# Kernel tuning notes

Measured on AMD Instinct MI355X. Metric: run time of the kernel, lower is better.

The kernel has to match this reference:

```python
import jax, jax.numpy as jnp
import numpy as np

N = 50000      # nodes
E = 800000     # edges (pos and neg each)
IN = 128       # in_channels
HID = 64       # hidden_dim
H = 4          # heads
OUT = 64       # out_channels


def setup_inputs() -> dict:
    key = jax.random.key(0)
    ks = jax.random.split(key, 11)
    s = 0.05
    return {
        "x": jax.random.normal(ks[0], (N, IN), dtype=jnp.float32),
        "pos_edge_index": jax.random.randint(ks[1], (2, E), 0, N, dtype=jnp.int32),
        "neg_edge_index": jax.random.randint(ks[2], (2, E), 0, N, dtype=jnp.int32),
        # conv1 params: Linear [IN, H*HID], attention vectors [H, HID], bias [H*HID]
        "W1": jax.random.normal(ks[3], (IN, H * HID), dtype=jnp.float32) * s,
        "att_src1": jax.random.normal(ks[4], (H, HID), dtype=jnp.float32) * s,
        "att_dst1": jax.random.normal(ks[5], (H, HID), dtype=jnp.float32) * s,
        "b1": jax.random.normal(ks[6], (H * HID,), dtype=jnp.float32) * s,
        # conv2 params: heads=1
        "W2": jax.random.normal(ks[7], (H * HID, OUT), dtype=jnp.float32) * s,
        "att_src2": jax.random.normal(ks[8], (1, OUT), dtype=jnp.float32) * s,
        "att_dst2": jax.random.normal(ks[9], (1, OUT), dtype=jnp.float32) * s,
        "b2": jax.random.normal(ks[10], (OUT,), dtype=jnp.float32) * s,
    }


def gat_conv(x, edge_index, W, att_src, att_dst, bias, heads, ch):
    """PyG GATConv: add self-loops, per-head linear, leaky-relu edge score,
    scatter-softmax over target neighborhoods, scatter-add aggregation."""
    n = x.shape[0]
    loop = jnp.arange(n, dtype=edge_index.dtype)
    src = jnp.concatenate([edge_index[0], loop])  # message source j
    dst = jnp.concatenate([edge_index[1], loop])  # aggregation target i

    h = (x @ W).reshape(n, heads, ch)                      # [N, H, C]
    a_s = jnp.einsum("nhc,hc->nh", h, att_src)             # alpha from source
    a_d = jnp.einsum("nhc,hc->nh", h, att_dst)             # alpha from target

    alpha = jax.nn.leaky_relu(a_s[src] + a_d[dst], 0.2)    # [Etot, H]
    m = jax.ops.segment_max(alpha, dst, num_segments=n)    # per-target max
    e = jnp.exp(alpha - m[dst])
    denom = jax.ops.segment_sum(e, dst, num_segments=n)
    w = e / (denom[dst] + 1e-16)                           # softmax weights

    out = jax.ops.segment_sum(w[:, :, None] * h[src], dst, num_segments=n)
    return out.reshape(n, heads * ch) + bias


def reference(x, pos_edge_index, neg_edge_index,
              W1, att_src1, att_dst1, b1,
              W2, att_src2, att_dst2, b2):
    # encode
    z = jax.nn.relu(gat_conv(x, pos_edge_index, W1, att_src1, att_dst1, b1, H, HID))
    z = gat_conv(z, pos_edge_index, W2, att_src2, att_dst2, b2, 1, OUT)
    # decode: edge dot-product logits over pos + neg edges
    ei = jnp.concatenate([pos_edge_index, neg_edge_index], axis=-1)  # [2, 2E]
    logits = (z[ei[0]] * z[ei[1]]).sum(axis=-1)                      # [2E]
    return logits
```

## Files before the change

### kernel.cpp

```cpp
#include <hip/hip_runtime.h>
#include <hip/hip_bf16.h>
#include <math.h>

#define IN_CH 128
#define HID 64
#define HEADS 4
#define C1 (HEADS*HID)
#define OUT_CH 64
#define NSL 64
#define MAXNH 25024

typedef __attribute__((ext_vector_type(8))) short short8v;
typedef __attribute__((ext_vector_type(4))) float f32x4;

__device__ __forceinline__ float lrelu(float x){ return x > 0.f ? x : 0.2f*x; }

__device__ __forceinline__ ushort f2b(float f){
  unsigned u = __builtin_bit_cast(unsigned, f);
  unsigned r = (u + 0x7FFF + ((u>>16)&1)) >> 16;
  return (ushort)r;
}
__device__ __forceinline__ float b2f(ushort b){
  unsigned u = ((unsigned)b) << 16;
  return __builtin_bit_cast(float, u);
}

__device__ __forceinline__ float wsum64(float v){
  #pragma unroll
  for (int m = 32; m >= 1; m >>= 1) v += __shfl_xor(v, m, 64);
  return v;
}

__device__ __forceinline__ float dot2(unsigned ua, unsigned ub){
  float la = __builtin_bit_cast(float, ua << 16);
  float ha = __builtin_bit_cast(float, ua & 0xFFFF0000u);
  float lb = __builtin_bit_cast(float, ub << 16);
  float hb = __builtin_bit_cast(float, ub & 0xFFFF0000u);
  return la*lb + ha*hb;
}

__device__ __forceinline__ void unpack8(uint4 u, float* v){
  v[0]=__builtin_bit_cast(float,u.x<<16); v[1]=__builtin_bit_cast(float,u.x&0xFFFF0000u);
  v[2]=__builtin_bit_cast(float,u.y<<16); v[3]=__builtin_bit_cast(float,u.y&0xFFFF0000u);
  v[4]=__builtin_bit_cast(float,u.z<<16); v[5]=__builtin_bit_cast(float,u.z&0xFFFF0000u);
  v[6]=__builtin_bit_cast(float,u.w<<16); v[7]=__builtin_bit_cast(float,u.w&0xFFFF0000u);
}


__global__ __launch_bounds__(1024) void k_hist2(
    const int* __restrict__ dst, unsigned* __restrict__ part, int e, int nh, int n){
  __shared__ unsigned hist[MAXNH];
  int b = blockIdx.x;
  int half = b >> 6, slice = b & (NSL-1);
  int base = half*nh;
  int cnt = half ? (n - nh) : nh;
  int tid = threadIdx.x;
  for (int i = tid; i < cnt; i += 1024) hist[i] = 0u;
  __syncthreads();
  int ES = (e + NSL - 1) / NSL;
  int es = slice*ES, ee = min(e, es + ES);
  for (int t = es + tid; t < ee; t += 1024){
    int d = dst[t];
    if (d >= base && d < base + cnt) atomicAdd(&hist[d - base], 1u);
  }
  __syncthreads();
  unsigned* pb = part + (size_t)b*nh;
  for (int i = tid; i < cnt; i += 1024) pb[i] = hist[i];
}

__global__ void k_degred(unsigned* __restrict__ part, int* __restrict__ deg,
                         int* __restrict__ bsum, int n, int nh){
  __shared__ int buf[256];
  int b = blockIdx.x, tid = threadIdx.x;
  int g = b*256 + tid;
  int dv = 0;
  if (g < n){
    int half = (g >= nh) ? 1 : 0;
    int i = g - half*nh;
    size_t base = (size_t)(half*NSL)*nh + i;
    unsigned run = 0;
    #pragma unroll 8
    for (int s = 0; s < NSL; ++s){
      unsigned v = part[base + (size_t)s*nh];
      part[base + (size_t)s*nh] = run;
      run += v;
    }
    dv = (int)run + 1;
    deg[g] = dv;
  }
  buf[tid] = dv;
  __syncthreads();
  for (int off = 128; off > 0; off >>= 1){
    if (tid < off) buf[tid] += buf[tid + off];
    __syncthreads();
  }
  if (tid == 0) bsum[b] = buf[0];
}

__global__ void k_scanb(int* bsum, int nb){
  __shared__ int buf[256];
  int tid = threadIdx.x;
  int v = (tid < nb) ? bsum[tid] : 0;
  buf[tid] = v;
  __syncthreads();
  for (int off = 1; off < 256; off <<= 1){
    int t = (tid >= off) ? buf[tid - off] : 0;
    __syncthreads();
    buf[tid] += t;
    __syncthreads();
  }
  if (tid < nb) bsum[tid] = buf[tid] - v;
}

__global__ void k_scanfinal(const int* __restrict__ deg, const int* __restrict__ bsum,
                            int* rowptr, ushort* csrc, int n){
  __shared__ int buf[256];
  int b = blockIdx.x, tid = threadIdx.x;
  int i = b*256 + tid;
  int v = (i < n) ? deg[i] : 0;
  buf[tid] = v;
  __syncthreads();
  for (int off = 1; off < 256; off <<= 1){
    int t = (tid >= off) ? buf[tid - off] : 0;
    __syncthreads();
    buf[tid] += t;
    __syncthreads();
  }
  if (i < n){
    int r = bsum[b] + buf[tid];
    rowptr[i + 1] = r;
    csrc[r - 1] = (ushort)i;
  }
  if (b == 0 && tid == 0) rowptr[0] = 0;
}

__global__ __launch_bounds__(1024) void k_scatter2(
    const int* __restrict__ src, const int* __restrict__ dst,
    const int* __restrict__ rowptr, const unsigned* __restrict__ part,
    ushort* __restrict__ csrc, int e, int nh, int n){
  __shared__ unsigned cur[MAXNH];
  int b = blockIdx.x;
  int half = b >> 6, slice = b & (NSL-1);
  int base = half*nh;
  int cnt = half ? (n - nh) : nh;
  int tid = threadIdx.x;
  const unsigned* pb = part + (size_t)b*nh;
  for (int i = tid; i < cnt; i += 1024)
    cur[i] = (unsigned)rowptr[base + i] + pb[i];
  __syncthreads();
  int ES = (e + NSL - 1) / NSL;
  int es = slice*ES, ee = min(e, es + ES);
  for (int t = es + tid; t < ee; t += 1024){
    int d = dst[t];
    if (d >= base && d < base + cnt){
      unsigned slot = atomicAdd(&cur[d - base], 1u);
      __builtin_nontemporal_store((ushort)src[t], csrc + slot);
    }
  }
}

__global__ void k_setup(const float* __restrict__ W1, ushort* __restrict__ W1t,
                        const float* __restrict__ W2, ushort* __restrict__ W2t,
                        const float* __restrict__ as1v, const float* __restrict__ ad1v,
                        const float* __restrict__ as2v, const float* __restrict__ ad2v,
                        float* was4, float* wad4, float* w2s, float* w2d){
  int b = blockIdx.x, tid = threadIdx.x;
  if (b < 128){
    int i = b*256 + tid;
    int k = i >> 8, c = i & 255;
    W1t[(size_t)c*IN_CH + k] = f2b(W1[i]);
  } else if (b < 192){
    int i = (b - 128)*256 + tid;
    int k = i >> 6, c = i & 63;
    W2t[(size_t)c*C1 + k] = f2b(W2[i]);
  } else if (b == 192){
    #pragma unroll
    for (int r = 0; r < 2; ++r){
      int t = tid + r*256;
      int c = t >> 2, h = t & 3;
      float s = 0.f, d = 0.f;
      for (int j = 0; j < HID; ++j){
        float w = W1[c*C1 + h*HID + j];
        s += w * as1v[h*HID + j];
        d += w * ad1v[h*HID + j];
      }
      was4[t] = s; wad4[t] = d;
    }
  } else {
    float s = 0.f, d = 0.f;
    for (int o = 0; o < OUT_CH; ++o){
      float w = W2[tid*OUT_CH + o];
      s += w * as2v[o];
      d += w * ad2v[o];
    }
    w2s[tid] = s; w2d[tid] = d;
  }
}

__global__ __launch_bounds__(256) void k_fattc(const float* __restrict__ x,
    const float* __restrict__ was4, const float* __restrict__ wad4,
    ushort* __restrict__ xb, float* __restrict__ as1, float* __restrict__ ad1, int n){
  int i = blockIdx.x*4 + (threadIdx.x >> 6);
  int l = threadIdx.x & 63;
  if (i >= n) return;
  float2 u = *(const float2*)(x + (size_t)i*IN_CH + 2*l);
  ushort2 o; o.x = f2b(u.x); o.y = f2b(u.y);
  *(ushort2*)(xb + (size_t)i*IN_CH + 2*l) = o;
  float v0 = u.x, v1 = u.y;
  f32x4 s0 = *(const f32x4*)(was4 + 8*l);
  f32x4 s1 = *(const f32x4*)(was4 + 8*l + 4);
  f32x4 d0 = *(const f32x4*)(wad4 + 8*l);
  f32x4 d1 = *(const f32x4*)(wad4 + 8*l + 4);
  f32x4 ps, pd;
  #pragma unroll
  for (int h = 0; h < 4; ++h){
    ps[h] = wsum64(v0*s0[h] + v1*s1[h]);
    pd[h] = wsum64(v0*d0[h] + v1*d1[h]);
  }
  if (l == 0){
    *(f32x4*)(as1 + 4*i) = ps;
    *(f32x4*)(ad1 + 4*i) = pd;
  }
}

__global__ __launch_bounds__(256) void k_fatt2(const ushort* __restrict__ z1b,
    const float* __restrict__ w2s, const float* __restrict__ w2d,
    float* __restrict__ as2, float* __restrict__ ad2, int n){
  int i = blockIdx.x*4 + (threadIdx.x >> 6);
  int l = threadIdx.x & 63;
  if (i >= n) return;
  ushort4 u = *(const ushort4*)(z1b + (size_t)i*C1 + 4*l);
  float v0 = b2f(u.x), v1 = b2f(u.y), v2 = b2f(u.z), v3 = b2f(u.w);
  f32x4 s = *(const f32x4*)(w2s + 4*l);
  f32x4 d = *(const f32x4*)(w2d + 4*l);
  float ps = wsum64(v0*s[0] + v1*s[1] + v2*s[2] + v3*s[3]);
  float pd = wsum64(v0*d[0] + v1*d[1] + v2*d[2] + v3*d[3]);
  if (l == 0){ as2[i] = ps; ad2[i] = pd; }
}

__global__ __launch_bounds__(64) void k_fagg1(
    const ushort* __restrict__ xb, const float* __restrict__ as1,
    const float* __restrict__ ad1, const int* __restrict__ rowptr,
    const ushort* __restrict__ csrc, ushort* __restrict__ xagg, int n)
{
  __shared__ float  s_w[4][4][17];
  __shared__ ushort s_src[4][16];
  int tid = threadIdx.x;
  int grp = tid >> 4, ln = tid & 15;
  int i = blockIdx.x*4 + grp;
  if (i >= n) return;
  int beg = rowptr[i], end = rowptr[i+1];
  f32x4 ad4 = *(const f32x4*)(ad1 + 4*i);

  f32x4 S = (f32x4)(0.f);
  f32x4 ev0 = (f32x4)(0.f), ev1 = (f32x4)(0.f);
  int sj0 = 0, sj1 = 0, it = 0;
  for (int sl = beg + ln; sl < end; sl += 16, ++it){
    int sj = csrc[sl];
    f32x4 a4 = *(const f32x4*)(as1 + 4*sj);
    f32x4 ev;
    #pragma unroll
    for (int h = 0; h < 4; ++h)
      ev[h] = __expf(fminf(lrelu(a4[h] + ad4[h]), 60.f));
    if (it == 0){ ev0 = ev; sj0 = sj; }
    else if (it == 1){ ev1 = ev; sj1 = sj; }
    #pragma unroll
    for (int h = 0; h < 4; ++h) S[h] += ev[h];
  }
  f32x4 rd;
  #pragma unroll
  for (int h = 0; h < 4; ++h){
    float sh = S[h];
    #pragma unroll
    for (int k = 8; k >= 1; k >>= 1) sh += __shfl_xor(sh, k, 16);
    rd[h] = 1.f/(sh + 1e-16f);
  }

  float acc[4][8] = {};
  int nch = (end - beg + 15) >> 4;
  for (int c = 0; c < nch; ++c){
    int cs = beg + c*16;
    int cn = min(16, end - cs);
    if (ln < cn){
      int sj; f32x4 ev;
      if (c == 0){ sj = sj0; ev = ev0; }
      else if (c == 1){ sj = sj1; ev = ev1; }
      else {
        sj = csrc[cs + ln];
        f32x4 a4 = *(const f32x4*)(as1 + 4*sj);
        #pragma unroll
        for (int h = 0; h < 4; ++h)
          ev[h] = __expf(fminf(lrelu(a4[h] + ad4[h]), 60.f));
      }
      s_src[grp][ln] = (ushort)sj;
      #pragma unroll
      for (int h = 0; h < 4; ++h)
        s_w[grp][h][ln] = ev[h] * rd[h];
    }
    int e = 0;
    if (cn >= 4){
      uint4 u0 = *(const uint4*)(xb + (size_t)s_src[grp][0]*IN_CH + ln*8);
      uint4 u1 = *(const uint4*)(xb + (size_t)s_src[grp][1]*IN_CH + ln*8);
      uint4 u2 = *(const uint4*)(xb + (size_t)s_src[grp][2]*IN_CH + ln*8);
      uint4 u3 = *(const uint4*)(xb + (size_t)s_src[grp][3]*IN_CH + ln*8);
      for (; e + 7 < cn; e += 4){
        uint4 n0 = *(const uint4*)(xb + (size_t)s_src[grp][e+4]*IN_CH + ln*8);
        uint4 n1 = *(const uint4*)(xb + (size_t)s_src[grp][e+5]*IN_CH + ln*8);
        uint4 n2 = *(const uint4*)(xb + (size_t)s_src[grp][e+6]*IN_CH + ln*8);
        uint4 n3 = *(const uint4*)(xb + (size_t)s_src[grp][e+7]*IN_CH + ln*8);
        float v0[8], v1[8], v2[8], v3[8];
        unpack8(u0, v0); unpack8(u1, v1); unpack8(u2, v2); unpack8(u3, v3);
        #pragma unroll
        for (int h = 0; h < 4; ++h){
          float w0 = s_w[grp][h][e],   w1 = s_w[grp][h][e+1];
          float w2 = s_w[grp][h][e+2], w3 = s_w[grp][h][e+3];
          #pragma unroll
          for (int cc = 0; cc < 8; ++cc)
            acc[h][cc] += w0*v0[cc] + w1*v1[cc] + w2*v2[cc] + w3*v3[cc];
        }
        u0 = n0; u1 = n1; u2 = n2; u3 = n3;
      }
      {
        float v0[8], v1[8], v2[8], v3[8];
        unpack8(u0, v0); unpack8(u1, v1); unpack8(u2, v2); unpack8(u3, v3);
        #pragma unroll
        for (int h = 0; h < 4; ++h){
          float w0 = s_w[grp][h][e],   w1 = s_w[grp][h][e+1];
          float w2 = s_w[grp][h][e+2], w3 = s_w[grp][h][e+3];
          #pragma unroll
          for (int cc = 0; cc < 8; ++cc)
            acc[h][cc] += w0*v0[cc] + w1*v1[cc] + w2*v2[cc] + w3*v3[cc];
        }
        e += 4;
      }
    }
    for (; e < cn; ++e){
      uint4 u = *(const uint4*)(xb + (size_t)s_src[grp][e]*IN_CH + ln*8);
      float v[8];
      unpack8(u, v);
      #pragma unroll
      for (int h = 0; h < 4; ++h){
        float w = s_w[grp][h][e];
        #pragma unroll
        for (int cc = 0; cc < 8; ++cc) acc[h][cc] += w*v[cc];
      }
    }
  }
  #pragma unroll
  for (int h = 0; h < 4; ++h){
    uint4 o;
    o.x = (unsigned)f2b(acc[h][0]) | ((unsigned)f2b(acc[h][1])<<16);
    o.y = (unsigned)f2b(acc[h][2]) | ((unsigned)f2b(acc[h][3])<<16);
    o.z = (unsigned)f2b(acc[h][4]) | ((unsigned)f2b(acc[h][5])<<16);
    o.w = (unsigned)f2b(acc[h][6]) | ((unsigned)f2b(acc[h][7])<<16);
    *(uint4*)(xagg + (size_t)i*512 + h*128 + ln*8) = o;
  }
}

__global__ __launch_bounds__(64) void k_fagg2(
    const ushort* __restrict__ h2b, const float* __restrict__ as2,
    const float* __restrict__ ad2, const int* __restrict__ rowptr,
    const ushort* __restrict__ csrc, const float* __restrict__ bias,
    ushort* __restrict__ z2b, int n)
{
  __shared__ float  s_w[4][17];
  __shared__ ushort s_src[4][16];
  int tid = threadIdx.x;
  int grp = tid >> 4, ln = tid & 15;
  int i = blockIdx.x*4 + grp;
  if (i >= n) return;
  int beg = rowptr[i], end = rowptr[i+1];
  float adv = ad2[i];

  float S = 0.f;
  float ev0 = 0.f, ev1 = 0.f;
  int sj0 = 0, sj1 = 0, it = 0;
  for (int sl = beg + ln; sl < end; sl += 16, ++it){
    int sj = csrc[sl];
    float ev = __expf(fminf(lrelu(as2[sj] + adv), 60.f));
    if (it == 0){ ev0 = ev; sj0 = sj; }
    else if (it == 1){ ev1 = ev; sj1 = sj; }
    S += ev;
  }
  #pragma unroll
  for (int k = 8; k >= 1; k >>= 1) S += __shfl_xor(S, k, 16);
  float rd = 1.f/(S + 1e-16f);

  float acc[4] = {};
  int nch = (end - beg + 15) >> 4;
  for (int c = 0; c < nch; ++c){
    int cs = beg + c*16;
    int cn = min(16, end - cs);
    if (ln < cn){
      int sj; float ev;
      if (c == 0){ sj = sj0; ev = ev0; }
      else if (c == 1){ sj = sj1; ev = ev1; }
      else { sj = csrc[cs + ln]; ev = __expf(fminf(lrelu(as2[sj] + adv), 60.f)); }
      s_src[grp][ln] = (ushort)sj;
      s_w[grp][ln] = ev * rd;
    }
    int e = 0;
    for (; e + 1 < cn; e += 2){
      int sjA = s_src[grp][e], sjB = s_src[grp][e+1];
      float wA = s_w[grp][e], wB = s_w[grp][e+1];
      ushort4 uA = *(const ushort4*)(h2b + (size_t)sjA*OUT_CH + ln*4);
      ushort4 uB = *(const ushort4*)(h2b + (size_t)sjB*OUT_CH + ln*4);
      acc[0] += wA*b2f(uA.x) + wB*b2f(uB.x);
      acc[1] += wA*b2f(uA.y) + wB*b2f(uB.y);
      acc[2] += wA*b2f(uA.z) + wB*b2f(uB.z);
      acc[3] += wA*b2f(uA.w) + wB*b2f(uB.w);
    }
    if (e < cn){
      int sj = s_src[grp][e];
      float w = s_w[grp][e];
      ushort4 u = *(const ushort4*)(h2b + (size_t)sj*OUT_CH + ln*4);
      acc[0] += w*b2f(u.x); acc[1] += w*b2f(u.y);
      acc[2] += w*b2f(u.z); acc[3] += w*b2f(u.w);
    }
  }
  ushort4 o;
  o.x = f2b(acc[0] + bias[ln*4]);
  o.y = f2b(acc[1] + bias[ln*4+1]);
  o.z = f2b(acc[2] + bias[ln*4+2]);
  o.w = f2b(acc[3] + bias[ln*4+3]);
  *(ushort4*)(z2b + (size_t)i*OUT_CH + ln*4) = o;
}

template<bool RELU_BIAS>
__global__ __launch_bounds__(256) void k_gemm2(
    const ushort* __restrict__ A, const ushort* __restrict__ Bt,
    ushort* __restrict__ Cb, const float* __restrict__ bias,
    int M, int K, int lda, int ldc, int aZ, int bZ, int cZ)
{
  constexpr int BM = 128, BN = 64, NF = 2;
  __shared__ uint4 As[BM*8];
  __shared__ uint4 Bs[BN*8];
  int tid = threadIdx.x;
  int wave = tid >> 6, lane = tid & 63;
  int wr = wave >> 1, wc = wave & 1;
  int bm = blockIdx.y * BM;
  int z = blockIdx.z;
  const ushort* Az = A + (size_t)z*aZ;
  const ushort* Bz = Bt + (size_t)z*bZ;
  int g = lane >> 4, lr = lane & 15;

  f32x4 acc[4][NF];
  #pragma unroll
  for (int m = 0; m < 4; ++m)
    #pragma unroll
    for (int n = 0; n < NF; ++n) acc[m][n] = (f32x4)(0.f);

  for (int k0 = 0; k0 < K; k0 += 64){
    for (int idx = tid; idx < BM*8; idx += 256){
      int r = idx >> 3, c = idx & 7;
      int gr = bm + r;
      uint4 v = make_uint4(0u,0u,0u,0u);
      if (gr < M) v = *(const uint4*)(Az + (size_t)gr*lda + k0 + c*8);
      As[r*8 + (c ^ (r & 7))] = v;
    }
    for (int idx = tid; idx < BN*8; idx += 256){
      int r = idx >> 3, c = idx & 7;
      uint4 v = *(const uint4*)(Bz + (size_t)r*K + k0 + c*8);
      Bs[r*8 + (c ^ (r & 7))] = v;
    }
    __syncthreads();
    #pragma unroll
    for (int kk = 0; kk < 2; ++kk){
      short8v af[4], bf[NF];
      #pragma unroll
      for (int m = 0; m < 4; ++m){
        int r = wr*64 + m*16 + lr;
        int c = kk*4 + g;
        af[m] = *(const short8v*)&As[r*8 + (c ^ (r & 7))];
      }
      #pragma unroll
      for (int n = 0; n < NF; ++n){
        int r = wc*32 + n*16 + lr;
        int c = kk*4 + g;
        bf[n] = *(const short8v*)&Bs[r*8 + (c ^ (r & 7))];
      }
      #pragma unroll
      for (int m = 0; m < 4; ++m)
        #pragma unroll
        for (int n = 0; n < NF; ++n)
          acc[m][n] = __builtin_amdgcn_mfma_f32_16x16x32_bf16(af[m], bf[n], acc[m][n], 0, 0, 0);
    }
    __syncthreads();
  }
  #pragma unroll
  for (int m = 0; m < 4; ++m){
    #pragma unroll
    for (int q = 0; q < 4; ++q){
      int row = bm + wr*64 + m*16 + g*4 + q;
      if (row < M){
        #pragma unroll
        for (int n = 0; n < NF; ++n){
          int col = wc*32 + n*16 + lr;
          float v = acc[m][n][q];
          if (RELU_BIAS) v = fmaxf(v + bias[cZ*z + col], 0.f);
          Cb[(size_t)row*ldc + cZ*z + col] = f2b(v);
        }
      }
    }
  }
}

__global__ void k_decode(const ushort* __restrict__ z2b, const int* __restrict__ pos,
                         const int* __restrict__ neg, float* __restrict__ out, int e){
  int g = blockIdx.x*256 + threadIdx.x;
  int hf = e >> 1;
  int k = g >> 3;
  int sub = g & 7;
  if (k >= hf) return;
  int a0 = __builtin_nontemporal_load(pos + k);
  int b0 = __builtin_nontemporal_load(pos + e + k);
  int a1 = __builtin_nontemporal_load(pos + k + hf);
  int b1 = __builtin_nontemporal_load(pos + e + k + hf);
  int a2 = __builtin_nontemporal_load(neg + k);
  int b2 = __builtin_nontemporal_load(neg + e + k);
  int a3 = __builtin_nontemporal_load(neg + k + hf);
  int b3 = __builtin_nontemporal_load(neg + e + k + hf);
  uint4 ua0 = *(const uint4*)(z2b + (size_t)a0*OUT_CH + sub*8);
  uint4 ub0 = *(const uint4*)(z2b + (size_t)b0*OUT_CH + sub*8);
  uint4 ua1 = *(const uint4*)(z2b + (size_t)a1*OUT_CH + sub*8);
  uint4 ub1 = *(const uint4*)(z2b + (size_t)b1*OUT_CH + sub*8);
  uint4 ua2 = *(const uint4*)(z2b + (size_t)a2*OUT_CH + sub*8);
  uint4 ub2 = *(const uint4*)(z2b + (size_t)b2*OUT_CH + sub*8);
  uint4 ua3 = *(const uint4*)(z2b + (size_t)a3*OUT_CH + sub*8);
  uint4 ub3 = *(const uint4*)(z2b + (size_t)b3*OUT_CH + sub*8);
  float p0 = dot2(ua0.x, ub0.x) + dot2(ua0.y, ub0.y) + dot2(ua0.z, ub0.z) + dot2(ua0.w, ub0.w);
  float p1 = dot2(ua1.x, ub1.x) + dot2(ua1.y, ub1.y) + dot2(ua1.z, ub1.z) + dot2(ua1.w, ub1.w);
  float p2 = dot2(ua2.x, ub2.x) + dot2(ua2.y, ub2.y) + dot2(ua2.z, ub2.z) + dot2(ua2.w, ub2.w);
  float p3 = dot2(ua3.x, ub3.x) + dot2(ua3.y, ub3.y) + dot2(ua3.z, ub3.z) + dot2(ua3.w, ub3.w);
  #pragma unroll
  for (int mm = 4; mm >= 1; mm >>= 1){
    p0 += __shfl_xor(p0, mm, 64);
    p1 += __shfl_xor(p1, mm, 64);
    p2 += __shfl_xor(p2, mm, 64);
    p3 += __shfl_xor(p3, mm, 64);
  }
  if (sub == 0){
    __builtin_nontemporal_store(p0, out + k);
    __builtin_nontemporal_store(p1, out + k + hf);
    __builtin_nontemporal_store(p2, out + e + k);
    __builtin_nontemporal_store(p3, out + e + k + hf);
  }
}

extern "C" void kernel_launch(void* const* d_in, const int* in_sizes, int n_in,
                              void* d_out, int out_size, void* d_ws, size_t ws_size,
                              hipStream_t stream) {
  const float* x        = (const float*)d_in[0];
  const int*   pos      = (const int*)d_in[1];
  const int*   neg      = (const int*)d_in[2];
  const float* W1       = (const float*)d_in[3];
  const float* att_src1 = (const float*)d_in[4];
  const float* att_dst1 = (const float*)d_in[5];
  const float* b1       = (const float*)d_in[6];
  const float* W2       = (const float*)d_in[7];
  const float* att_src2 = (const float*)d_in[8];
  const float* att_dst2 = (const float*)d_in[9];
  const float* b2       = (const float*)d_in[10];
  float* out = (float*)d_out;

  const int N = in_sizes[0] / IN_CH;
  const int E = in_sizes[1] / 2;
  const int NNZ = E + N;
  const int NH = (N + 1) / 2;

  char* w = (char*)d_ws;
  ushort* xb   = (ushort*)w;  w += (size_t)N*IN_CH*2;
  ushort* xagg = (ushort*)w;  w += (size_t)N*512*2;
  ushort* z1b  = (ushort*)w;  w += (size_t)N*C1*2;
  float* as1   = (float*)w;   w += (size_t)N*4*4;
  float* ad1   = (float*)w;   w += (size_t)N*4*4;
  float* as2   = (float*)w;   w += (size_t)N*4;
  float* ad2   = (float*)w;   w += (size_t)N*4;
  ushort* W1t  = (ushort*)w;  w += (size_t)C1*IN_CH*2;
  ushort* W2t  = (ushort*)w;  w += (size_t)OUT_CH*C1*2;
  float* was4  = (float*)w;   w += 512*4;
  float* wad4  = (float*)w;   w += 512*4;
  float* w2s   = (float*)w;   w += 256*4;
  float* w2d   = (float*)w;   w += 256*4;
  int* deg     = (int*)w;     w += (size_t)N*4;
  int* rowptr  = (int*)w;     w += (size_t)(N+1)*4;
  int* bsum    = (int*)w;     w += (size_t)256*4;
  unsigned* part = (unsigned*)w; w += (size_t)2*NSL*NH*4;
  ushort* csrc = (ushort*)w;  w += (size_t)NNZ*2;

  ushort* h2b = xagg;
  ushort* z2b = xagg + (size_t)N*OUT_CH;

  int nb = (N + 255)/256;
  const int* pdst = pos + E;

  k_setup<<<194, 256, 0, stream>>>(W1, W1t, W2, W2t,
      att_src1, att_dst1, att_src2, att_dst2, was4, wad4, w2s, w2d);
  k_hist2<<<2*NSL, 1024, 0, stream>>>(pdst, part, E, NH, N);
  k_degred<<<nb, 256, 0, stream>>>(part, deg, bsum, N, NH);
  k_fattc<<<(N + 3)/4, 256, 0, stream>>>(x, was4, wad4, xb, as1, ad1, N);
  k_scanb<<<1, 256, 0, stream>>>(bsum, nb);
  k_scanfinal<<<nb, 256, 0, stream>>>(deg, bsum, rowptr, csrc, N);
  k_scatter2<<<2*NSL, 1024, 0, stream>>>(pos, pdst, rowptr, part, csrc, E, NH, N);

  k_fagg1<<<(N + 3)/4, 64, 0, stream>>>(xb, as1, ad1, rowptr, csrc, xagg, N);

  {
    dim3 g(1, (N + 127)/128, 4);
    k_gemm2<true><<<g, 256, 0, stream>>>(xagg, W1t, z1b, b1,
        N, IN_CH, 512, C1, IN_CH, OUT_CH*IN_CH, OUT_CH);
  }
  k_fatt2<<<(N + 3)/4, 256, 0, stream>>>(z1b, w2s, w2d, as2, ad2, N);

  {
    dim3 g(1, (N + 127)/128, 1);
    k_gemm2<false><<<g, 256, 0, stream>>>(z1b, W2t, h2b, nullptr,
        N, C1, C1, OUT_CH, 0, 0, 0);
  }
  k_fagg2<<<(N + 3)/4, 64, 0, stream>>>(h2b, as2, ad2, rowptr, csrc, b2, z2b, N);

  int db = (int)(((size_t)(E/2)*8 + 255)/256);
  k_decode<<<db, 256, 0, stream>>>(z2b, pos, neg, out, E);
}
```

Before: 243.6 us.

## Split CSR build into quarter-node partitions, fold block scan, prefetch agg loads

The histogram and scatter kernels now split the node range into four quarters instead of two. This shrinks each block's shared-memory table, which should allow more resident blocks, and doubles the block count. The separate single-block scan of block sums is removed: each scanfinal block now sums the preceding block totals itself, which saves a kernel launch at the cost of redundant reads. The second-layer aggregation loop software-pipelines its gathered feature loads one pair ahead to hide memory latency. A side effect is that every edge is now read by four blocks instead of two.

Result: no change. 240.0 us (-1.5%).

```diff
diff --git a/kernel.cpp b/kernel.cpp
--- a/kernel.cpp
+++ b/kernel.cpp
@@ -8,7 +8,8 @@
 #define C1 (HEADS*HID)
 #define OUT_CH 64
 #define NSL 64
-#define MAXNH 25024
+#define NQ 4
+#define MAXNQ 12512
 
 typedef __attribute__((ext_vector_type(8))) short short8v;
 typedef __attribute__((ext_vector_type(4))) float f32x4;
@@ -48,12 +49,12 @@
 
 
 __global__ __launch_bounds__(1024) void k_hist2(
-    const int* __restrict__ dst, unsigned* __restrict__ part, int e, int nh, int n){
-  __shared__ unsigned hist[MAXNH];
+    const int* __restrict__ dst, unsigned* __restrict__ part, int e, int nq, int n){
+  __shared__ unsigned hist[MAXNQ];
   int b = blockIdx.x;
-  int half = b >> 6, slice = b & (NSL-1);
-  int base = half*nh;
-  int cnt = half ? (n - nh) : nh;
+  int q = b >> 6, slice = b & (NSL-1);
+  int base = q*nq;
+  int cnt = min(nq, n - base);
   int tid = threadIdx.x;
   for (int i = tid; i < cnt; i += 1024) hist[i] = 0u;
   __syncthreads();
@@ -64,25 +65,25 @@
     if (d >= base && d < base + cnt) atomicAdd(&hist[d - base], 1u);
   }
   __syncthreads();
-  unsigned* pb = part + (size_t)b*nh;
+  unsigned* pb = part + (size_t)b*nq;
   for (int i = tid; i < cnt; i += 1024) pb[i] = hist[i];
 }
 
 __global__ void k_degred(unsigned* __restrict__ part, int* __restrict__ deg,
-                         int* __restrict__ bsum, int n, int nh){
+                         int* __restrict__ bsum, int n, int nq){
   __shared__ int buf[256];
   int b = blockIdx.x, tid = threadIdx.x;
   int g = b*256 + tid;
   int dv = 0;
   if (g < n){
-    int half = (g >= nh) ? 1 : 0;
-    int i = g - half*nh;
-    size_t base = (size_t)(half*NSL)*nh + i;
+    int q = g / nq;
+    int i = g - q*nq;
+    size_t base = (size_t)(q*NSL)*nq + i;
     unsigned run = 0;
     #pragma unroll 8
     for (int s = 0; s < NSL; ++s){
-      unsigned v = part[base + (size_t)s*nh];
-      part[base + (size_t)s*nh] = run;
+      unsigned v = part[base + (size_t)s*nq];
+      part[base + (size_t)s*nq] = run;
       run += v;
     }
     dv = (int)run + 1;
@@ -97,25 +98,23 @@
   if (tid == 0) bsum[b] = buf[0];
 }
 
-__global__ void k_scanb(int* bsum, int nb){
-  __shared__ int buf[256];
-  int tid = threadIdx.x;
-  int v = (tid < nb) ? bsum[tid] : 0;
-  buf[tid] = v;
-  __syncthreads();
-  for (int off = 1; off < 256; off <<= 1){
-    int t = (tid >= off) ? buf[tid - off] : 0;
-    __syncthreads();
-    buf[tid] += t;
-    __syncthreads();
-  }
-  if (tid < nb) bsum[tid] = buf[tid] - v;
-}
-
 __global__ void k_scanfinal(const int* __restrict__ deg, const int* __restrict__ bsum,
                             int* rowptr, ushort* csrc, int n){
   __shared__ int buf[256];
+  __shared__ int s_base;
   int b = blockIdx.x, tid = threadIdx.x;
+  int part = 0;
+  for (int s = tid; s < b; s += 256) part += bsum[s];
+  buf[tid] = part;
+  __syncthreads();
+  for (int off = 128; off > 0; off >>= 1){
+    if (tid < off) buf[tid] += buf[tid + off];
+    __syncthreads();
+  }
+  if (tid == 0) s_base = buf[0];
+  __syncthreads();
+  int base = s_base;
+
   int i = b*256 + tid;
   int v = (i < n) ? deg[i] : 0;
   buf[tid] = v;
@@ -127,7 +126,7 @@
     __syncthreads();
   }
   if (i < n){
-    int r = bsum[b] + buf[tid];
+    int r = base + buf[tid];
     rowptr[i + 1] = r;
     csrc[r - 1] = (ushort)i;
   }
@@ -137,14 +136,14 @@
 __global__ __launch_bounds__(1024) void k_scatter2(
     const int* __restrict__ src, const int* __restrict__ dst,
     const int* __restrict__ rowptr, const unsigned* __restrict__ part,
-    ushort* __restrict__ csrc, int e, int nh, int n){
-  __shared__ unsigned cur[MAXNH];
+    ushort* __restrict__ csrc, int e, int nq, int n){
+  __shared__ unsigned cur[MAXNQ];
   int b = blockIdx.x;
-  int half = b >> 6, slice = b & (NSL-1);
-  int base = half*nh;
-  int cnt = half ? (n - nh) : nh;
+  int q = b >> 6, slice = b & (NSL-1);
+  int base = q*nq;
+  int cnt = min(nq, n - base);
   int tid = threadIdx.x;
-  const unsigned* pb = part + (size_t)b*nh;
+  const unsigned* pb = part + (size_t)b*nq;
   for (int i = tid; i < cnt; i += 1024)
     cur[i] = (unsigned)rowptr[base + i] + pb[i];
   __syncthreads();
@@ -400,15 +399,27 @@
       s_w[grp][ln] = ev * rd;
     }
     int e = 0;
-    for (; e + 1 < cn; e += 2){
-      int sjA = s_src[grp][e], sjB = s_src[grp][e+1];
-      float wA = s_w[grp][e], wB = s_w[grp][e+1];
-      ushort4 uA = *(const ushort4*)(h2b + (size_t)sjA*OUT_CH + ln*4);
-      ushort4 uB = *(const ushort4*)(h2b + (size_t)sjB*OUT_CH + ln*4);
-      acc[0] += wA*b2f(uA.x) + wB*b2f(uB.x);
-      acc[1] += wA*b2f(uA.y) + wB*b2f(uB.y);
-      acc[2] += wA*b2f(uA.z) + wB*b2f(uB.z);
-      acc[3] += wA*b2f(uA.w) + wB*b2f(uB.w);
+    if (cn >= 2){
+      ushort4 uA = *(const ushort4*)(h2b + (size_t)s_src[grp][0]*OUT_CH + ln*4);
+      ushort4 uB = *(const ushort4*)(h2b + (size_t)s_src[grp][1]*OUT_CH + ln*4);
+      for (; e + 3 < cn; e += 2){
+        ushort4 uC = *(const ushort4*)(h2b + (size_t)s_src[grp][e+2]*OUT_CH + ln*4);
+        ushort4 uD = *(const ushort4*)(h2b + (size_t)s_src[grp][e+3]*OUT_CH + ln*4);
+        float wA = s_w[grp][e], wB = s_w[grp][e+1];
+        acc[0] += wA*b2f(uA.x) + wB*b2f(uB.x);
+        acc[1] += wA*b2f(uA.y) + wB*b2f(uB.y);
+        acc[2] += wA*b2f(uA.z) + wB*b2f(uB.z);
+        acc[3] += wA*b2f(uA.w) + wB*b2f(uB.w);
+        uA = uC; uB = uD;
+      }
+      {
+        float wA = s_w[grp][e], wB = s_w[grp][e+1];
+        acc[0] += wA*b2f(uA.x) + wB*b2f(uB.x);
+        acc[1] += wA*b2f(uA.y) + wB*b2f(uB.y);
+        acc[2] += wA*b2f(uA.z) + wB*b2f(uB.z);
+        acc[3] += wA*b2f(uA.w) + wB*b2f(uB.w);
+        e += 2;
+      }
     }
     if (e < cn){
       int sj = s_src[grp][e];
@@ -566,7 +577,7 @@
   const int N = in_sizes[0] / IN_CH;
   const int E = in_sizes[1] / 2;
   const int NNZ = E + N;
-  const int NH = (N + 1) / 2;
+  const int NQ4 = (N + NQ - 1) / NQ;
 
   char* w = (char*)d_ws;
   ushort* xb   = (ushort*)w;  w += (size_t)N*IN_CH*2;
@@ -585,7 +596,7 @@
   int* deg     = (int*)w;     w += (size_t)N*4;
   int* rowptr  = (int*)w;     w += (size_t)(N+1)*4;
   int* bsum    = (int*)w;     w += (size_t)256*4;
-  unsigned* part = (unsigned*)w; w += (size_t)2*NSL*NH*4;
+  unsigned* part = (unsigned*)w; w += (size_t)NQ*NSL*NQ4*4;
   ushort* csrc = (ushort*)w;  w += (size_t)NNZ*2;
 
   ushort* h2b = xagg;
@@ -596,12 +607,11 @@
 
   k_setup<<<194, 256, 0, stream>>>(W1, W1t, W2, W2t,
       att_src1, att_dst1, att_src2, att_dst2, was4, wad4, w2s, w2d);
-  k_hist2<<<2*NSL, 1024, 0, stream>>>(pdst, part, E, NH, N);
-  k_degred<<<nb, 256, 0, stream>>>(part, deg, bsum, N, NH);
+  k_hist2<<<NQ*NSL, 1024, 0, stream>>>(pdst, part, E, NQ4, N);
+  k_degred<<<nb, 256, 0, stream>>>(part, deg, bsum, N, NQ4);
   k_fattc<<<(N + 3)/4, 256, 0, stream>>>(x, was4, wad4, xb, as1, ad1, N);
-  k_scanb<<<1, 256, 0, stream>>>(bsum, nb);
   k_scanfinal<<<nb, 256, 0, stream>>>(deg, bsum, rowptr, csrc, N);
-  k_scatter2<<<2*NSL, 1024, 0, stream>>>(pos, pdst, rowptr, part, csrc, E, NH, N);
+  k_scatter2<<<NQ*NSL, 1024, 0, stream>>>(pos, pdst, rowptr, part, csrc, E, NQ4, N);
 
   k_fagg1<<<(N + 3)/4, 64, 0, stream>>>(xb, as1, ad1, rowptr, csrc, xagg, N);
 
```
